# Kernel optimization log

Measured on AMD Instinct MI355X. Metric: run time of the kernel, lower is better.

Reference implementation:

```python
import jax, jax.numpy as jnp
import numpy as np

T, H, E, F, K, FS = 2048, 2048, 64, 512, 8, 512


def setup_inputs() -> dict:
    key = jax.random.key(0)
    ks = jax.random.split(key, 6)
    s = 0.02
    return {
        "hidden_states": jax.random.normal(ks[0], (T, H), jnp.float32),
        # merged gate: E router logits + 1 shared-expert gate logit
        "W_gate": jax.random.normal(ks[1], (H, E + 1), jnp.float32) * s,
        # per-expert merged gate_up proj: [E, H, 2F]
        "W_gate_up": jax.random.normal(ks[2], (E, H, 2 * F), jnp.float32) * s,
        "W_down": jax.random.normal(ks[3], (E, F, H), jnp.float32) * s,
        # shared expert
        "Ws_gate_up": jax.random.normal(ks[4], (H, 2 * FS), jnp.float32) * s,
        "Ws_down": jax.random.normal(ks[5], (FS, H), jnp.float32) * s,
    }


def reference(hidden_states, W_gate, W_gate_up, W_down, Ws_gate_up, Ws_down):
    x = hidden_states  # [T, H]
    logits_all = x @ W_gate                      # [T, E+1]
    router_logits = logits_all[:, :E]
    shared_gate_logit = logits_all[:, E:]        # [T, 1]

    # FusedMoE routing: softmax -> top_k -> renormalize (norm_topk_prob=True)
    probs = jax.nn.softmax(router_logits.astype(jnp.float32), axis=-1)
    topk_w, topk_idx = jax.lax.top_k(probs, K)   # [T, K]
    topk_w = topk_w / jnp.sum(topk_w, axis=-1, keepdims=True)
    # dense combine weights [T, E] (zero for unselected experts)
    combine = jnp.zeros((T, E), probs.dtype).at[
        jnp.arange(T)[:, None], topk_idx].set(topk_w)

    # grouped expert GEMMs (dense reference: every expert sees all tokens,
    # combine-weights zero-out unrouted pairs)
    gu = jnp.einsum('th,ehf->etf', x, W_gate_up)   # [E, T, 2F]
    g, u = jnp.split(gu, 2, axis=-1)
    act = jax.nn.silu(g) * u                       # [E, T, F]
    # apply combine weight before down-proj to avoid [E, T, H] intermediate
    act = act * combine.T[:, :, None].astype(act.dtype)
    routed = jnp.einsum('etf,efh->th', act, W_down)  # [T, H]

    # shared expert (Qwen3NextMLP with sigmoid expert_gate)
    sgu = x @ Ws_gate_up                           # [T, 2FS]
    sg, su = jnp.split(sgu, 2, axis=-1)
    shared = (jax.nn.silu(sg) * su) @ Ws_down      # [T, H]
    shared = jax.nn.sigmoid(shared_gate_logit) * shared

    return shared + routed.astype(x.dtype)
```

## Files before the change

### kernel.cpp

```cpp
#include <hip/hip_runtime.h>
#include <hip/hip_bf16.h>
#include <math.h>

#define T_TOK 2048
#define H_DIM 2048
#define E_NUM 64
#define F_DIM 512
#define K_TOP 8
#define FS_DIM 512
#define NROWS (T_TOK * K_TOP)

typedef __attribute__((ext_vector_type(8))) short short8v;
typedef __attribute__((ext_vector_type(4))) float f32x4;

static __device__ __forceinline__ unsigned short f2bf(float f) {
    unsigned int u = __float_as_uint(f);
    u += 0x7fff + ((u >> 16) & 1);
    return (unsigned short)(u >> 16);
}

__global__ __launch_bounds__(256) void cvt_bf16_kernel(
    const float* __restrict__ in, unsigned short* __restrict__ out, int n8)
{
    int i = blockIdx.x * 256 + threadIdx.x;
    if (i < n8) {
        const float4* p = (const float4*)(in + (size_t)i * 8);
        float4 v0 = p[0], v1 = p[1];
        ushort4 a = make_ushort4(f2bf(v0.x), f2bf(v0.y), f2bf(v0.z), f2bf(v0.w));
        ushort4 b = make_ushort4(f2bf(v1.x), f2bf(v1.y), f2bf(v1.z), f2bf(v1.w));
        ushort4* q = (ushort4*)(out + (size_t)i * 8);
        q[0] = a; q[1] = b;
    }
}

__global__ __launch_bounds__(64) void router_kernel(
    const float* __restrict__ x, const float* __restrict__ Wg,
    int* __restrict__ topk_idx, float* __restrict__ topk_w,
    float* __restrict__ sgate, int* __restrict__ counts)
{
    const int t = blockIdx.x;
    const int lane = threadIdx.x;
    const float* xr = x + (size_t)t * H_DIM;

    float a0 = 0.f, a1 = 0.f, a2 = 0.f, a3 = 0.f;
    for (int h = 0; h < H_DIM; h += 4) {
        float4 xv = *(const float4*)&xr[h];
        a0 += xv.x * Wg[(h + 0) * 65 + lane];
        a1 += xv.y * Wg[(h + 1) * 65 + lane];
        a2 += xv.z * Wg[(h + 2) * 65 + lane];
        a3 += xv.w * Wg[(h + 3) * 65 + lane];
    }
    float logit = (a0 + a1) + (a2 + a3);

    float a64 = 0.f;
    for (int h = lane; h < H_DIM; h += 64) a64 += xr[h] * Wg[h * 65 + 64];
#pragma unroll
    for (int off = 32; off >= 1; off >>= 1) a64 += __shfl_xor(a64, off);

    float v = logit;
    float selv[K_TOP]; int seli[K_TOP];
#pragma unroll
    for (int k = 0; k < K_TOP; ++k) {
        float mv = v; int mi = lane;
#pragma unroll
        for (int off = 32; off >= 1; off >>= 1) {
            float ov = __shfl_xor(mv, off);
            int   oi = __shfl_xor(mi, off);
            if (ov > mv || (ov == mv && oi < mi)) { mv = ov; mi = oi; }
        }
        selv[k] = mv; seli[k] = mi;
        if (lane == mi) v = -INFINITY;
    }

    if (lane == 0) {
        float m = selv[0];
        float w[K_TOP]; float s = 0.f;
#pragma unroll
        for (int k = 0; k < K_TOP; ++k) { w[k] = __expf(selv[k] - m); s += w[k]; }
        float inv = 1.f / s;
#pragma unroll
        for (int k = 0; k < K_TOP; ++k) {
            topk_idx[t * K_TOP + k] = seli[k];
            topk_w[t * K_TOP + k] = w[k] * inv;
            atomicAdd(&counts[seli[k]], 1);
        }
        sgate[t] = 1.f / (1.f + __expf(-a64));
    }
}

__global__ __launch_bounds__(256) void bucket_kernel(
    const int* __restrict__ topk_idx, const float* __restrict__ topk_w,
    const int* __restrict__ counts, int* __restrict__ offsets,
    int* __restrict__ bucket_tok, float* __restrict__ bucket_w)
{
    const int e = blockIdx.x, thr = threadIdx.x;
    __shared__ int cnt[256];
    __shared__ int base_s;
    const int q0 = thr * 64;
    int c = 0;
    for (int q = 0; q < 64; ++q) c += (topk_idx[q0 + q] == e) ? 1 : 0;
    cnt[thr] = c;
    __syncthreads();
    if (thr == 0) {
        int off = 0;
        for (int i = 0; i < e; ++i) off += counts[i];
        offsets[e] = off;
        base_s = off;
        int run = 0;
        for (int i = 0; i < 256; ++i) { int tval = cnt[i]; cnt[i] = run; run += tval; }
    }
    __syncthreads();
    int pos = base_s + cnt[thr];
    for (int q = 0; q < 64; ++q) {
        int pp = q0 + q;
        if (topk_idx[pp] == e) {
            bucket_tok[pos] = pp >> 3;
            bucket_w[pos] = topk_w[pp];
            ++pos;
        }
    }
}

template<int FM, bool ROUTED>
__global__ __launch_bounds__(512, 4) void gu_mfma_kernel(
    const unsigned short* __restrict__ xb,
    const float* __restrict__ Wall,
    const int* __restrict__ counts, const int* __restrict__ offsets,
    const int* __restrict__ bucket_tok, const float* __restrict__ bucket_w,
    unsigned short* __restrict__ actout)
{
    constexpr int BM = FM * 64;
    constexpr int BST = 72;
    __shared__ __align__(16) unsigned short Bs[2][64 * BST];
    __shared__ int   toksS[BM];
    __shared__ float twsS[BM];

    const int tid  = threadIdx.x;
    const int lane = tid & 63;
    const int wid  = tid >> 6;
    const int wm = wid >> 1, wn = wid & 1;
    const int lrow = lane & 15, lhi = lane >> 4;

    int cblk, ne, base;
    const float* W;
    if (ROUTED) {
        int nw = (blockIdx.x & 7) * ((int)gridDim.x >> 3) + (blockIdx.x >> 3);
        int e = nw >> 4; cblk = nw & 15;
        ne = counts[e]; base = offsets[e];
        W = Wall + (size_t)e * H_DIM * (2 * F_DIM);
    } else {
        cblk = blockIdx.x;
        ne = T_TOK; base = 0;
        W = Wall;
    }
    const int c0 = cblk * 32;

    const int n4 = (tid & 15) * 4;
    const int kb = (tid >> 4) * 2;
    const int n5 = n4 & 31;
    const int wcol = ((n5 < 16) ? 0 : (F_DIM - 16)) + c0 + (n4 >> 5) * 16 + n5;

    const int m0_beg = ROUTED ? 0 : blockIdx.y * BM;
    const int m0_end = ROUTED ? ne : m0_beg + BM;

    for (int m0 = m0_beg; m0 < m0_end; m0 += BM) {
        __syncthreads();
        for (int i = tid; i < BM; i += 512) {
            if (ROUTED) {
                int idx = m0 + i; bool v = idx < ne;
                toksS[i] = v ? bucket_tok[base + idx] : bucket_tok[base];
                twsS[i]  = v ? bucket_w[base + idx] : 0.f;
            } else {
                toksS[i] = m0 + i; twsS[i] = 1.f;
            }
        }
        __syncthreads();

        const unsigned short* aptr[FM];
#pragma unroll
        for (int fm = 0; fm < FM; ++fm) {
            int r = wm * (FM * 16) + fm * 16 + lrow;
            aptr[fm] = xb + (size_t)toksS[r] * H_DIM;
        }

        f32x4 acc[FM][2];
#pragma unroll
        for (int i = 0; i < FM; ++i) {
            acc[i][0] = (f32x4){0.f, 0.f, 0.f, 0.f};
            acc[i][1] = (f32x4){0.f, 0.f, 0.f, 0.f};
        }

        {
            float4 b0 = *(const float4*)&W[(size_t)kb * (2 * F_DIM) + wcol];
            float4 b1 = *(const float4*)&W[(size_t)(kb + 1) * (2 * F_DIM) + wcol];
#pragma unroll
            for (int cc = 0; cc < 4; ++cc) {
                ushort2 pk = make_ushort2(f2bf(((const float*)&b0)[cc]),
                                          f2bf(((const float*)&b1)[cc]));
                *(ushort2*)&Bs[0][(n4 + cc) * BST + kb] = pk;
            }
        }
        __syncthreads();

        const int NT = H_DIM / 64;
        for (int kt = 0; kt < NT; ++kt) {
            const int k0 = kt * 64;
            const unsigned short* curB = Bs[kt & 1];
            unsigned short* nxtB = Bs[(kt & 1) ^ 1];

            short8v a[2][FM];
#pragma unroll
            for (int ks = 0; ks < 2; ++ks)
#pragma unroll
                for (int fm = 0; fm < FM; ++fm)
                    a[ks][fm] = *(const short8v*)(aptr[fm] + k0 + (ks * 4 + lhi) * 8);

            float4 b0, b1;
            if (kt + 1 < NT) {
                b0 = *(const float4*)&W[(size_t)(k0 + 64 + kb) * (2 * F_DIM) + wcol];
                b1 = *(const float4*)&W[(size_t)(k0 + 64 + kb + 1) * (2 * F_DIM) + wcol];
            }

#pragma unroll
            for (int ks = 0; ks < 2; ++ks) {
                const int kc = ks * 4 + lhi;
                short8v bg = *(const short8v*)&curB[(wn * 32 + lrow) * BST + kc * 8];
                short8v bu = *(const short8v*)&curB[(wn * 32 + 16 + lrow) * BST + kc * 8];
#pragma unroll
                for (int fm = 0; fm < FM; ++fm) {
                    acc[fm][0] = __builtin_amdgcn_mfma_f32_16x16x32_bf16(a[ks][fm], bg, acc[fm][0], 0, 0, 0);
                    acc[fm][1] = __builtin_amdgcn_mfma_f32_16x16x32_bf16(a[ks][fm], bu, acc[fm][1], 0, 0, 0);
                }
            }

            if (kt + 1 < NT) {
#pragma unroll
                for (int cc = 0; cc < 4; ++cc) {
                    ushort2 pk = make_ushort2(f2bf(((const float*)&b0)[cc]),
                                              f2bf(((const float*)&b1)[cc]));
                    *(ushort2*)&nxtB[(n4 + cc) * BST + kb] = pk;
                }
            }
            __syncthreads();
        }

        const int acol = c0 + wn * 16 + lrow;
#pragma unroll
        for (int fm = 0; fm < FM; ++fm) {
#pragma unroll
            for (int i = 0; i < 4; ++i) {
                int ml = wm * (FM * 16) + fm * 16 + lhi * 4 + i;
                int idx = m0 + ml;
                if (!ROUTED || idx < ne) {
                    float gv = acc[fm][0][i], uv = acc[fm][1][i];
                    float s = gv / (1.f + __expf(-gv));
                    float val = s * uv * twsS[ml];
                    size_t orow = ROUTED ? (size_t)(base + idx) : (size_t)idx;
                    actout[orow * F_DIM + acol] = f2bf(val);
                }
            }
        }
    }
}

template<int FM, bool ROUTED>
__global__ __launch_bounds__(512, 4) void down_mfma_kernel(
    const unsigned short* __restrict__ actb,
    const float* __restrict__ Wall,
    const int* __restrict__ counts, const int* __restrict__ offsets,
    const int* __restrict__ bucket_tok, const float* __restrict__ sgate,
    float* __restrict__ out)
{
    constexpr int BM = FM * 64;
    constexpr int BST = 72;
    __shared__ __align__(16) unsigned short Bs[2][64 * BST];
    __shared__ int   toksS[BM];
    __shared__ float sgS[BM];

    const int tid  = threadIdx.x;
    const int lane = tid & 63;
    const int wid  = tid >> 6;
    const int wm = wid >> 1, wn = wid & 1;
    const int lrow = lane & 15, lhi = lane >> 4;

    int cblk, ne, base;
    const float* W;
    if (ROUTED) {
        int nw = (blockIdx.x & 7) * ((int)gridDim.x >> 3) + (blockIdx.x >> 3);
        int e = nw >> 5; cblk = nw & 31;
        ne = counts[e]; base = offsets[e];
        W = Wall + (size_t)e * F_DIM * H_DIM;
    } else {
        cblk = blockIdx.x;
        ne = T_TOK; base = 0;
        W = Wall;
    }
    const int c0 = cblk * 64;

    const int n4 = (tid & 15) * 4;
    const int kb = (tid >> 4) * 2;
    const int wcol = c0 + n4;

    const int m0_beg = ROUTED ? 0 : blockIdx.y * BM;
    const int m0_end = ROUTED ? ne : m0_beg + BM;

    for (int m0 = m0_beg; m0 < m0_end; m0 += BM) {
        __syncthreads();
        for (int i = tid; i < BM; i += 512) {
            if (ROUTED) {
                int idx = m0 + i;
                toksS[i] = (idx < ne) ? bucket_tok[base + idx] : 0;
            } else {
                sgS[i] = sgate[m0 + i];
            }
        }
        __syncthreads();

        const unsigned short* aptr[FM];
#pragma unroll
        for (int fm = 0; fm < FM; ++fm) {
            int r = wm * (FM * 16) + fm * 16 + lrow;
            int grow = ROUTED ? min(base + m0 + r, NROWS - 1) : (m0 + r);
            aptr[fm] = actb + (size_t)grow * F_DIM;
        }

        f32x4 acc[FM][2];
#pragma unroll
        for (int i = 0; i < FM; ++i) {
            acc[i][0] = (f32x4){0.f, 0.f, 0.f, 0.f};
            acc[i][1] = (f32x4){0.f, 0.f, 0.f, 0.f};
        }

        {
            float4 b0 = *(const float4*)&W[(size_t)kb * H_DIM + wcol];
            float4 b1 = *(const float4*)&W[(size_t)(kb + 1) * H_DIM + wcol];
#pragma unroll
            for (int cc = 0; cc < 4; ++cc) {
                ushort2 pk = make_ushort2(f2bf(((const float*)&b0)[cc]),
                                          f2bf(((const float*)&b1)[cc]));
                *(ushort2*)&Bs[0][(n4 + cc) * BST + kb] = pk;
            }
        }
        __syncthreads();

        const int NT = F_DIM / 64;
        for (int kt = 0; kt < NT; ++kt) {
            const int k0 = kt * 64;
            const unsigned short* curB = Bs[kt & 1];
            unsigned short* nxtB = Bs[(kt & 1) ^ 1];

            short8v a[2][FM];
#pragma unroll
            for (int ks = 0; ks < 2; ++ks)
#pragma unroll
                for (int fm = 0; fm < FM; ++fm)
                    a[ks][fm] = *(const short8v*)(aptr[fm] + k0 + (ks * 4 + lhi) * 8);

            float4 b0, b1;
            if (kt + 1 < NT) {
                b0 = *(const float4*)&W[(size_t)(k0 + 64 + kb) * H_DIM + wcol];
                b1 = *(const float4*)&W[(size_t)(k0 + 64 + kb + 1) * H_DIM + wcol];
            }

#pragma unroll
            for (int ks = 0; ks < 2; ++ks) {
                const int kc = ks * 4 + lhi;
                short8v bf0 = *(const short8v*)&curB[(wn * 32 + lrow) * BST + kc * 8];
                short8v bf1 = *(const short8v*)&curB[(wn * 32 + 16 + lrow) * BST + kc * 8];
#pragma unroll
                for (int fm = 0; fm < FM; ++fm) {
                    acc[fm][0] = __builtin_amdgcn_mfma_f32_16x16x32_bf16(a[ks][fm], bf0, acc[fm][0], 0, 0, 0);
                    acc[fm][1] = __builtin_amdgcn_mfma_f32_16x16x32_bf16(a[ks][fm], bf1, acc[fm][1], 0, 0, 0);
                }
            }

            if (kt + 1 < NT) {
#pragma unroll
                for (int cc = 0; cc < 4; ++cc) {
                    ushort2 pk = make_ushort2(f2bf(((const float*)&b0)[cc]),
                                              f2bf(((const float*)&b1)[cc]));
                    *(ushort2*)&nxtB[(n4 + cc) * BST + kb] = pk;
                }
            }
            __syncthreads();
        }

#pragma unroll
        for (int fm = 0; fm < FM; ++fm) {
#pragma unroll
            for (int fn = 0; fn < 2; ++fn) {
                int col = c0 + wn * 32 + fn * 16 + lrow;
#pragma unroll
                for (int i = 0; i < 4; ++i) {
                    int ml = wm * (FM * 16) + fm * 16 + lhi * 4 + i;
                    int idx = m0 + ml;
                    if (ROUTED) {
                        if (idx < ne)
                            atomicAdd(&out[(size_t)toksS[ml] * H_DIM + col], acc[fm][fn][i]);
                    } else {
                        out[(size_t)idx * H_DIM + col] = sgS[ml] * acc[fm][fn][i];
                    }
                }
            }
        }
    }
}

extern "C" void kernel_launch(void* const* d_in, const int* in_sizes, int n_in,
                              void* d_out, int out_size, void* d_ws, size_t ws_size,
                              hipStream_t stream) {
    const float* x    = (const float*)d_in[0];
    const float* Wg   = (const float*)d_in[1];
    const float* Wgu  = (const float*)d_in[2];
    const float* Wd   = (const float*)d_in[3];
    const float* Wsgu = (const float*)d_in[4];
    const float* Wsd  = (const float*)d_in[5];
    float* out = (float*)d_out;

    char* p = (char*)d_ws;
    auto alloc = [&](size_t bytes) {
        char* r = p;
        p += (bytes + 255) & ~(size_t)255;
        return r;
    };
    int*   topk_idx   = (int*)  alloc((size_t)T_TOK * K_TOP * sizeof(int));
    float* topk_w     = (float*)alloc((size_t)T_TOK * K_TOP * sizeof(float));
    float* sgate      = (float*)alloc((size_t)T_TOK * sizeof(float));
    int*   counts     = (int*)  alloc((size_t)E_NUM * sizeof(int));
    int*   offsets    = (int*)  alloc((size_t)E_NUM * sizeof(int));
    int*   bucket_tok = (int*)  alloc((size_t)NROWS * sizeof(int));
    float* bucket_w   = (float*)alloc((size_t)NROWS * sizeof(float));
    unsigned short* xb    = (unsigned short*)alloc((size_t)T_TOK * H_DIM * sizeof(short));
    unsigned short* act_r = (unsigned short*)alloc((size_t)NROWS * F_DIM * sizeof(short));
    unsigned short* act_s = (unsigned short*)alloc((size_t)T_TOK * FS_DIM * sizeof(short));

    hipMemsetAsync(counts, 0, E_NUM * sizeof(int), stream);
    cvt_bf16_kernel<<<(T_TOK * H_DIM / 8 + 255) / 256, 256, 0, stream>>>(x, xb, T_TOK * H_DIM / 8);
    router_kernel<<<T_TOK, 64, 0, stream>>>(x, Wg, topk_idx, topk_w, sgate, counts);
    bucket_kernel<<<E_NUM, 256, 0, stream>>>(topk_idx, topk_w, counts, offsets, bucket_tok, bucket_w);

    gu_mfma_kernel<5, true><<<16 * E_NUM, 512, 0, stream>>>(
        xb, Wgu, counts, offsets, bucket_tok, bucket_w, act_r);
    gu_mfma_kernel<2, false><<<dim3(16, T_TOK / 128), 512, 0, stream>>>(
        xb, Wsgu, counts, offsets, bucket_tok, bucket_w, act_s);

    down_mfma_kernel<2, false><<<dim3(32, T_TOK / 128), 512, 0, stream>>>(
        act_s, Wsd, counts, offsets, bucket_tok, sgate, out);
    down_mfma_kernel<5, true><<<32 * E_NUM, 512, 0, stream>>>(
        act_r, Wd, counts, offsets, bucket_tok, sgate, out);
}
```

Before: 817.7 us.

## Swizzle LDS B tiles and deepen weight prefetch pipeline in MoE GEMMs

After: 810.4 us. Within noise of the previous version (-0.9%).

```diff
diff --git a/kernel.cpp b/kernel.cpp
--- a/kernel.cpp
+++ b/kernel.cpp
@@ -18,6 +18,13 @@
     u += 0x7fff + ((u >> 16) & 1);
     return (unsigned short)(u >> 16);
 }
+
+#define BCHUNK(row, k8) ((((k8) ^ ((row) + ((row) >> 3)))) & 7)
+
+#define PIPE_BARRIER() do { \
+    asm volatile("s_waitcnt lgkmcnt(0)" ::: "memory"); \
+    __builtin_amdgcn_s_barrier(); \
+} while (0)
 
 __global__ __launch_bounds__(256) void cvt_bf16_kernel(
     const float* __restrict__ in, unsigned short* __restrict__ out, int n8)
@@ -130,8 +137,7 @@
     unsigned short* __restrict__ actout)
 {
     constexpr int BM = FM * 64;
-    constexpr int BST = 72;
-    __shared__ __align__(16) unsigned short Bs[2][64 * BST];
+    __shared__ __align__(16) unsigned short Bs[2][64 * 64];
     __shared__ int   toksS[BM];
     __shared__ float twsS[BM];
 
@@ -160,6 +166,21 @@
     const int n5 = n4 & 31;
     const int wcol = ((n5 < 16) ? 0 : (F_DIM - 16)) + c0 + (n4 >> 5) * 16 + n5;
 
+    int wr_off[4];
+#pragma unroll
+    for (int cc = 0; cc < 4; ++cc) {
+        int n = n4 + cc;
+        wr_off[cc] = n * 64 + BCHUNK(n, kb >> 3) * 8 + (kb & 7);
+    }
+    const int rg = wn * 32 + lrow, ru = wn * 32 + 16 + lrow;
+    int rd_g[2], rd_u[2];
+#pragma unroll
+    for (int ks = 0; ks < 2; ++ks) {
+        int kc = ks * 4 + lhi;
+        rd_g[ks] = rg * 64 + BCHUNK(rg, kc) * 8;
+        rd_u[ks] = ru * 64 + BCHUNK(ru, kc) * 8;
+    }
+
     const int m0_beg = ROUTED ? 0 : blockIdx.y * BM;
     const int m0_end = ROUTED ? ne : m0_beg + BM;
 
@@ -190,58 +211,58 @@
             acc[i][1] = (f32x4){0.f, 0.f, 0.f, 0.f};
         }
 
+        const int NT = H_DIM / 64;
+        float4 b0 = *(const float4*)&W[(size_t)kb * (2 * F_DIM) + wcol];
+        float4 b1 = *(const float4*)&W[(size_t)(kb + 1) * (2 * F_DIM) + wcol];
+#pragma unroll
+        for (int cc = 0; cc < 4; ++cc)
+            *(ushort2*)&Bs[0][wr_off[cc]] = make_ushort2(
+                f2bf(((const float*)&b0)[cc]), f2bf(((const float*)&b1)[cc]));
+        b0 = *(const float4*)&W[(size_t)(64 + kb) * (2 * F_DIM) + wcol];
+        b1 = *(const float4*)&W[(size_t)(64 + kb + 1) * (2 * F_DIM) + wcol];
+        PIPE_BARRIER();
+
+        for (int kt = 0; kt < NT - 1; ++kt) {
+            const int k0 = kt * 64;
+            unsigned short* nxtB = Bs[(kt & 1) ^ 1];
+#pragma unroll
+            for (int cc = 0; cc < 4; ++cc)
+                *(ushort2*)&nxtB[wr_off[cc]] = make_ushort2(
+                    f2bf(((const float*)&b0)[cc]), f2bf(((const float*)&b1)[cc]));
+            if (kt < NT - 2) {
+                b0 = *(const float4*)&W[(size_t)(k0 + 128 + kb) * (2 * F_DIM) + wcol];
+                b1 = *(const float4*)&W[(size_t)(k0 + 128 + kb + 1) * (2 * F_DIM) + wcol];
+            }
+            const unsigned short* curB = Bs[kt & 1];
+#pragma unroll
+            for (int ks = 0; ks < 2; ++ks) {
+                short8v bg = *(const short8v*)&curB[rd_g[ks]];
+                short8v bu = *(const short8v*)&curB[rd_u[ks]];
+                const int koff = k0 + (ks * 4 + lhi) * 8;
+#pragma unroll
+                for (int fm = 0; fm < FM; ++fm) {
+                    short8v af = *(const short8v*)(aptr[fm] + koff);
+                    acc[fm][0] = __builtin_amdgcn_mfma_f32_16x16x32_bf16(af, bg, acc[fm][0], 0, 0, 0);
+                    acc[fm][1] = __builtin_amdgcn_mfma_f32_16x16x32_bf16(af, bu, acc[fm][1], 0, 0, 0);
+                }
+            }
+            PIPE_BARRIER();
+        }
         {
-            float4 b0 = *(const float4*)&W[(size_t)kb * (2 * F_DIM) + wcol];
-            float4 b1 = *(const float4*)&W[(size_t)(kb + 1) * (2 * F_DIM) + wcol];
-#pragma unroll
-            for (int cc = 0; cc < 4; ++cc) {
-                ushort2 pk = make_ushort2(f2bf(((const float*)&b0)[cc]),
-                                          f2bf(((const float*)&b1)[cc]));
-                *(ushort2*)&Bs[0][(n4 + cc) * BST + kb] = pk;
-            }
-        }
-        __syncthreads();
-
-        const int NT = H_DIM / 64;
-        for (int kt = 0; kt < NT; ++kt) {
-            const int k0 = kt * 64;
-            const unsigned short* curB = Bs[kt & 1];
-            unsigned short* nxtB = Bs[(kt & 1) ^ 1];
-
-            short8v a[2][FM];
-#pragma unroll
-            for (int ks = 0; ks < 2; ++ks)
-#pragma unroll
-                for (int fm = 0; fm < FM; ++fm)
-                    a[ks][fm] = *(const short8v*)(aptr[fm] + k0 + (ks * 4 + lhi) * 8);
-
-            float4 b0, b1;
-            if (kt + 1 < NT) {
-                b0 = *(const float4*)&W[(size_t)(k0 + 64 + kb) * (2 * F_DIM) + wcol];
-                b1 = *(const float4*)&W[(size_t)(k0 + 64 + kb + 1) * (2 * F_DIM) + wcol];
-            }
-
+            const int k0 = (NT - 1) * 64;
+            const unsigned short* curB = Bs[(NT - 1) & 1];
 #pragma unroll
             for (int ks = 0; ks < 2; ++ks) {
-                const int kc = ks * 4 + lhi;
-                short8v bg = *(const short8v*)&curB[(wn * 32 + lrow) * BST + kc * 8];
-                short8v bu = *(const short8v*)&curB[(wn * 32 + 16 + lrow) * BST + kc * 8];
+                short8v bg = *(const short8v*)&curB[rd_g[ks]];
+                short8v bu = *(const short8v*)&curB[rd_u[ks]];
+                const int koff = k0 + (ks * 4 + lhi) * 8;
 #pragma unroll
                 for (int fm = 0; fm < FM; ++fm) {
-                    acc[fm][0] = __builtin_amdgcn_mfma_f32_16x16x32_bf16(a[ks][fm], bg, acc[fm][0], 0, 0, 0);
-                    acc[fm][1] = __builtin_amdgcn_mfma_f32_16x16x32_bf16(a[ks][fm], bu, acc[fm][1], 0, 0, 0);
-                }
-            }
-
-            if (kt + 1 < NT) {
-#pragma unroll
-                for (int cc = 0; cc < 4; ++cc) {
-                    ushort2 pk = make_ushort2(f2bf(((const float*)&b0)[cc]),
-                                              f2bf(((const float*)&b1)[cc]));
-                    *(ushort2*)&nxtB[(n4 + cc) * BST + kb] = pk;
-                }
-            }
-            __syncthreads();
+                    short8v af = *(const short8v*)(aptr[fm] + koff);
+                    acc[fm][0] = __builtin_amdgcn_mfma_f32_16x16x32_bf16(af, bg, acc[fm][0], 0, 0, 0);
+                    acc[fm][1] = __builtin_amdgcn_mfma_f32_16x16x32_bf16(af, bu, acc[fm][1], 0, 0, 0);
+                }
+            }
         }
 
         const int acol = c0 + wn * 16 + lrow;
@@ -272,8 +293,7 @@
     float* __restrict__ out)
 {
     constexpr int BM = FM * 64;
-    constexpr int BST = 72;
-    __shared__ __align__(16) unsigned short Bs[2][64 * BST];
+    __shared__ __align__(16) unsigned short Bs[2][64 * 64];
     __shared__ int   toksS[BM];
     __shared__ float sgS[BM];
 
@@ -301,6 +321,21 @@
     const int kb = (tid >> 4) * 2;
     const int wcol = c0 + n4;
 
+    int wr_off[4];
+#pragma unroll
+    for (int cc = 0; cc < 4; ++cc) {
+        int n = n4 + cc;
+        wr_off[cc] = n * 64 + BCHUNK(n, kb >> 3) * 8 + (kb & 7);
+    }
+    const int r0 = wn * 32 + lrow, r1 = wn * 32 + 16 + lrow;
+    int rd_0[2], rd_1[2];
+#pragma unroll
+    for (int ks = 0; ks < 2; ++ks) {
+        int kc = ks * 4 + lhi;
+        rd_0[ks] = r0 * 64 + BCHUNK(r0, kc) * 8;
+        rd_1[ks] = r1 * 64 + BCHUNK(r1, kc) * 8;
+    }
+
     const int m0_beg = ROUTED ? 0 : blockIdx.y * BM;
     const int m0_end = ROUTED ? ne : m0_beg + BM;
 
@@ -331,58 +366,58 @@
             acc[i][1] = (f32x4){0.f, 0.f, 0.f, 0.f};
         }
 
+        const int NT = F_DIM / 64;
+        float4 b0 = *(const float4*)&W[(size_t)kb * H_DIM + wcol];
+        float4 b1 = *(const float4*)&W[(size_t)(kb + 1) * H_DIM + wcol];
+#pragma unroll
+        for (int cc = 0; cc < 4; ++cc)
+            *(ushort2*)&Bs[0][wr_off[cc]] = make_ushort2(
+                f2bf(((const float*)&b0)[cc]), f2bf(((const float*)&b1)[cc]));
+        b0 = *(const float4*)&W[(size_t)(64 + kb) * H_DIM + wcol];
+        b1 = *(const float4*)&W[(size_t)(64 + kb + 1) * H_DIM + wcol];
+        PIPE_BARRIER();
+
+        for (int kt = 0; kt < NT - 1; ++kt) {
+            const int k0 = kt * 64;
+            unsigned short* nxtB = Bs[(kt & 1) ^ 1];
+#pragma unroll
+            for (int cc = 0; cc < 4; ++cc)
+                *(ushort2*)&nxtB[wr_off[cc]] = make_ushort2(
+                    f2bf(((const float*)&b0)[cc]), f2bf(((const float*)&b1)[cc]));
+            if (kt < NT - 2) {
+                b0 = *(const float4*)&W[(size_t)(k0 + 128 + kb) * H_DIM + wcol];
+                b1 = *(const float4*)&W[(size_t)(k0 + 128 + kb + 1) * H_DIM + wcol];
+            }
+            const unsigned short* curB = Bs[kt & 1];
+#pragma unroll
+            for (int ks = 0; ks < 2; ++ks) {
+                short8v bf0 = *(const short8v*)&curB[rd_0[ks]];
+                short8v bf1 = *(const short8v*)&curB[rd_1[ks]];
+                const int koff = k0 + (ks * 4 + lhi) * 8;
+#pragma unroll
+                for (int fm = 0; fm < FM; ++fm) {
+                    short8v af = *(const short8v*)(aptr[fm] + koff);
+                    acc[fm][0] = __builtin_amdgcn_mfma_f32_16x16x32_bf16(af, bf0, acc[fm][0], 0, 0, 0);
+                    acc[fm][1] = __builtin_amdgcn_mfma_f32_16x16x32_bf16(af, bf1, acc[fm][1], 0, 0, 0);
+                }
+            }
+            PIPE_BARRIER();
+        }
         {
-            float4 b0 = *(const float4*)&W[(size_t)kb * H_DIM + wcol];
-            float4 b1 = *(const float4*)&W[(size_t)(kb + 1) * H_DIM + wcol];
-#pragma unroll
-            for (int cc = 0; cc < 4; ++cc) {
-                ushort2 pk = make_ushort2(f2bf(((const float*)&b0)[cc]),
-                                          f2bf(((const float*)&b1)[cc]));
-                *(ushort2*)&Bs[0][(n4 + cc) * BST + kb] = pk;
-            }
-        }
-        __syncthreads();
-
-        const int NT = F_DIM / 64;
-        for (int kt = 0; kt < NT; ++kt) {
-            const int k0 = kt * 64;
-            const unsigned short* curB = Bs[kt & 1];
-            unsigned short* nxtB = Bs[(kt & 1) ^ 1];
-
-            short8v a[2][FM];
-#pragma unroll
-            for (int ks = 0; ks < 2; ++ks)
-#pragma unroll
-                for (int fm = 0; fm < FM; ++fm)
-                    a[ks][fm] = *(const short8v*)(aptr[fm] + k0 + (ks * 4 + lhi) * 8);
-
-            float4 b0, b1;
-            if (kt + 1 < NT) {
-                b0 = *(const float4*)&W[(size_t)(k0 + 64 + kb) * H_DIM + wcol];
-                b1 = *(const float4*)&W[(size_t)(k0 + 64 + kb + 1) * H_DIM + wcol];
-            }
-
+            const int k0 = (NT - 1) * 64;
+            const unsigned short* curB = Bs[(NT - 1) & 1];
 #pragma unroll
             for (int ks = 0; ks < 2; ++ks) {
-                const int kc = ks * 4 + lhi;
-                short8v bf0 = *(const short8v*)&curB[(wn * 32 + lrow) * BST + kc * 8];
-                short8v bf1 = *(const short8v*)&curB[(wn * 32 + 16 + lrow) * BST + kc * 8];
+                short8v bf0 = *(const short8v*)&curB[rd_0[ks]];
+                short8v bf1 = *(const short8v*)&curB[rd_1[ks]];
+                const int koff = k0 + (ks * 4 + lhi) * 8;
 #pragma unroll
                 for (int fm = 0; fm < FM; ++fm) {
-                    acc[fm][0] = __builtin_amdgcn_mfma_f32_16x16x32_bf16(a[ks][fm], bf0, acc[fm][0], 0, 0, 0);
-                    acc[fm][1] = __builtin_amdgcn_mfma_f32_16x16x32_bf16(a[ks][fm], bf1, acc[fm][1], 0, 0, 0);
-                }
-            }
-
-            if (kt + 1 < NT) {
-#pragma unroll
-                for (int cc = 0; cc < 4; ++cc) {
-                    ushort2 pk = make_ushort2(f2bf(((const float*)&b0)[cc]),
-                                              f2bf(((const float*)&b1)[cc]));
-                    *(ushort2*)&nxtB[(n4 + cc) * BST + kb] = pk;
-                }
-            }
-            __syncthreads();
+                    short8v af = *(const short8v*)(aptr[fm] + koff);
+                    acc[fm][0] = __builtin_amdgcn_mfma_f32_16x16x32_bf16(af, bf0, acc[fm][0], 0, 0, 0);
+                    acc[fm][1] = __builtin_amdgcn_mfma_f32_16x16x32_bf16(af, bf1, acc[fm][1], 0, 0, 0);
+                }
+            }
         }
 
 #pragma unroll
```
